# Optimization experiments

Measured on AMD Instinct MI355X. Metric: run time of the kernel, lower is better.

The kernel has to match this reference:

```python
import jax, jax.numpy as jnp
import numpy as np

BS, TS, H = 16, 2048, 1024
MT_LEN = TS // 2  # static split point; matches first_sentence_mask built in setup_inputs
SCALE = 1.0 / float(np.sqrt(H))
NEG = -10000.0


def masked_average(x, mask):
    # x: (bs, ts, h), mask: (bs, ts) -> (bs, h)
    m = mask[..., None].astype(x.dtype)
    return (x * m).sum(1) / m.sum(1)


def setup_inputs() -> dict:
    key = jax.random.key(0)
    ks = jax.random.split(key, 8)
    hidden_states = jax.random.normal(ks[0], (BS, TS, H), jnp.float32)
    embeddings = jax.random.normal(ks[1], (BS, TS, H), jnp.float32)
    attention_mask = jnp.ones((BS, TS), jnp.int32)
    first_sentence_mask = jnp.concatenate(
        [jnp.ones((BS, MT_LEN), jnp.int32), jnp.zeros((BS, TS - MT_LEN), jnp.int32)], axis=1)
    first_piece_mask = jnp.ones((BS, TS), jnp.int32)  # unused (aggregation='none')
    s = 1.0 / float(np.sqrt(H))
    Wq = jax.random.normal(ks[2], (H, H), jnp.float32) * s
    bq = jnp.zeros((H,), jnp.float32)
    Wk = jax.random.normal(ks[3], (H, H), jnp.float32) * s
    bk = jnp.zeros((H,), jnp.float32)
    Wv = jax.random.normal(ks[4], (H, H), jnp.float32) * s
    bv = jnp.zeros((H,), jnp.float32)
    return dict(hidden_states=hidden_states, embeddings=embeddings,
                attention_mask=attention_mask, first_sentence_mask=first_sentence_mask,
                first_piece_mask=first_piece_mask,
                Wq=Wq, bq=bq, Wk=Wk, bk=bk, Wv=Wv, bv=bv)


def reference(hidden_states, embeddings, attention_mask, first_sentence_mask,
              first_piece_mask, Wq, bq, Wk, bk, Wv, bv):
    # alpha_merge < 0, squared_attn=False, kv_rep='embeddings', alpha=1.0 (softmax)
    kv_rep = embeddings
    hidden_states_avg = masked_average(hidden_states, attention_mask)   # (bs, h)
    q = hidden_states_avg @ Wq.T + bq                                   # (bs, h)
    k = kv_rep @ Wk.T + bk                                              # (bs, ts, h)
    v = kv_rep @ Wv.T + bv                                              # (bs, ts, h)
    scores = jnp.einsum('bh,bth->bt', q, k) * SCALE                     # (bs, ts)
    scores = jnp.where(attention_mask.astype(bool), scores, NEG)
    probas = jax.nn.softmax(scores, axis=-1)                            # (bs, ts)
    combined_summary = jnp.einsum('bt,bth->bh', probas, v)              # (bs, h)
    # separate_mt_and_src on probas (static split at MT_LEN)
    mt_mask = attention_mask[:, :MT_LEN] * first_sentence_mask[:, :MT_LEN]
    src_mask = attention_mask[:, MT_LEN:] * (1 - first_sentence_mask[:, MT_LEN:])
    mt_probas = probas[:, :MT_LEN] * mt_mask.astype(probas.dtype)
    src_probas = probas[:, MT_LEN:] * src_mask.astype(probas.dtype)
    return combined_summary, mt_probas, src_probas
```

## Files before the change

kernel.cpp:

```cpp
#include <hip/hip_runtime.h>

#define BS 16
#define TS 2048
#define H 1024
#define MT_LEN 1024
#define NCHUNK 64
#define CHUNK_T (TS / NCHUNK)
#define SCALE 0.03125f
#define NEG -10000.0f

__global__ __launch_bounds__(256)
void k1_hidden_partial(const float* __restrict__ hs,
                       const int* __restrict__ am,
                       float* __restrict__ pA) {
    const int c = blockIdx.x, b = blockIdx.y;
    const int tid = threadIdx.x;
    const int h4 = tid * 4;
    __shared__ float ms[CHUNK_T];
    if (tid < CHUNK_T) ms[tid] = (float)am[b * TS + c * CHUNK_T + tid];
    __syncthreads();
    const float* base = hs + ((size_t)(b * TS + c * CHUNK_T)) * H + h4;
    float4 acc = {0.f, 0.f, 0.f, 0.f};
#pragma unroll 4
    for (int t = 0; t < CHUNK_T; ++t) {
        const float m = ms[t];
        float4 v = *(const float4*)(base + (size_t)t * H);
        acc.x += m * v.x; acc.y += m * v.y; acc.z += m * v.z; acc.w += m * v.w;
    }
    *(float4*)(pA + ((size_t)(b * NCHUNK + c)) * H + h4) = acc;
}

__global__ __launch_bounds__(256)
void k2_avg(const float* __restrict__ pA, const int* __restrict__ am,
            float* __restrict__ avg) {
    const int b = blockIdx.x;
    const int tid = threadIdx.x;
    __shared__ float red[256];
    int s = 0;
    for (int t = tid; t < TS; t += 256) s += am[b * TS + t];
    red[tid] = (float)s;
    __syncthreads();
    for (int o = 128; o > 0; o >>= 1) { if (tid < o) red[tid] += red[tid + o]; __syncthreads(); }
    const float inv = 1.0f / red[0];
    const int h4 = tid * 4;
    float4 acc = {0.f, 0.f, 0.f, 0.f};
    for (int c = 0; c < NCHUNK; ++c) {
        float4 v = *(const float4*)(pA + ((size_t)(b * NCHUNK + c)) * H + h4);
        acc.x += v.x; acc.y += v.y; acc.z += v.z; acc.w += v.w;
    }
    acc.x *= inv; acc.y *= inv; acc.z *= inv; acc.w *= inv;
    *(float4*)(avg + (size_t)b * H + h4) = acc;
}

__global__ __launch_bounds__(256)
void k3_q(const float* __restrict__ avg, const float* __restrict__ Wq,
          const float* __restrict__ bq, float* __restrict__ q) {
    const int b = blockIdx.y;
    const int tid = threadIdx.x;
    __shared__ float avs[H];
    *(float4*)(&avs[tid * 4]) = *(const float4*)(avg + (size_t)b * H + tid * 4);
    __syncthreads();
    const int wave = tid >> 6, lane = tid & 63;
    const int i = blockIdx.x * 4 + wave;
    const float* row = Wq + (size_t)i * H;
    float acc = 0.f;
#pragma unroll
    for (int u = 0; u < 4; ++u) {
        const int j = u * 256 + lane * 4;
        float4 w = *(const float4*)(row + j);
        float4 a = *(const float4*)(&avs[j]);
        acc += w.x * a.x + w.y * a.y + w.z * a.z + w.w * a.w;
    }
#pragma unroll
    for (int o = 32; o > 0; o >>= 1) acc += __shfl_xor(acc, o);
    if (lane == 0) q[b * H + i] = acc + bq[i];
}

__global__ __launch_bounds__(256)
void k4_qkp(const float* __restrict__ q, const float* __restrict__ Wk,
            const float* __restrict__ bk, float* __restrict__ qk_p,
            float* __restrict__ qbk_p) {
    const int ic = blockIdx.x, b = blockIdx.y;
    const int tid = threadIdx.x;
    __shared__ float qs[256];
    __shared__ float red[256];
    qs[tid] = q[b * H + ic * 256 + tid];
    __syncthreads();
    const int j = tid * 4;
    float4 acc = {0.f, 0.f, 0.f, 0.f};
#pragma unroll 8
    for (int ii = 0; ii < 256; ++ii) {
        const float s = qs[ii];
        float4 w = *(const float4*)(Wk + ((size_t)(ic * 256 + ii)) * H + j);
        acc.x += s * w.x; acc.y += s * w.y; acc.z += s * w.z; acc.w += s * w.w;
    }
    *(float4*)(qk_p + ((size_t)(ic * BS + b)) * H + j) = acc;
    red[tid] = qs[tid] * bk[ic * 256 + tid];
    __syncthreads();
    for (int o = 128; o > 0; o >>= 1) { if (tid < o) red[tid] += red[tid + o]; __syncthreads(); }
    if (tid == 0) qbk_p[ic * BS + b] = red[0];
}

__global__ __launch_bounds__(256)
void k5_fused(const float* __restrict__ emb, const int* __restrict__ am,
              const float* __restrict__ qk_p, const float* __restrict__ qbk_p,
              float* __restrict__ scores, float* __restrict__ mc_arr,
              float* __restrict__ zc_arr, float* __restrict__ e_c) {
    const int c = blockIdx.x, b = blockIdx.y;
    const int tid = threadIdx.x;
    __shared__ float qks[H];
    __shared__ float sbuf[CHUNK_T];
    __shared__ float wbuf[CHUNK_T];
    {
        const int j = tid * 4;
        float4 a = {0.f, 0.f, 0.f, 0.f};
#pragma unroll
        for (int ic = 0; ic < 4; ++ic) {
            float4 v = *(const float4*)(qk_p + ((size_t)(ic * BS + b)) * H + j);
            a.x += v.x; a.y += v.y; a.z += v.z; a.w += v.w;
        }
        *(float4*)(&qks[j]) = a;
    }
    const float qb = qbk_p[0 * BS + b] + qbk_p[1 * BS + b] + qbk_p[2 * BS + b] + qbk_p[3 * BS + b];
    __syncthreads();
    const int wave = tid >> 6, lane = tid & 63;
    for (int tt = 0; tt < 8; ++tt) {
        const int tl = wave * 8 + tt;
        const int t = c * CHUNK_T + tl;
        const float* e = emb + ((size_t)(b * TS + t)) * H;
        float acc = 0.f;
#pragma unroll
        for (int u = 0; u < 4; ++u) {
            const int j = u * 256 + lane * 4;
            float4 v = *(const float4*)(e + j);
            float4 a = *(const float4*)(&qks[j]);
            acc += v.x * a.x + v.y * a.y + v.z * a.z + v.w * a.w;
        }
#pragma unroll
        for (int o = 32; o > 0; o >>= 1) acc += __shfl_xor(acc, o);
        if (lane == 0) {
            const float sc = (am[b * TS + t] != 0) ? (acc + qb) * SCALE : NEG;
            scores[b * TS + t] = sc;
            sbuf[tl] = sc;
        }
    }
    __syncthreads();
    float mc = -3.4e38f;
#pragma unroll
    for (int tl = 0; tl < CHUNK_T; ++tl) mc = fmaxf(mc, sbuf[tl]);
    if (tid < CHUNK_T) wbuf[tid] = __expf(sbuf[tid] - mc);
    __syncthreads();
    float zc = 0.f;
#pragma unroll
    for (int tl = 0; tl < CHUNK_T; ++tl) zc += wbuf[tl];
    const int h4 = tid * 4;
    const float* base = emb + ((size_t)(b * TS + c * CHUNK_T)) * H + h4;
    float4 acc = {0.f, 0.f, 0.f, 0.f};
#pragma unroll 4
    for (int t = 0; t < CHUNK_T; ++t) {
        const float p = wbuf[t];
        float4 v = *(const float4*)(base + (size_t)t * H);
        acc.x += p * v.x; acc.y += p * v.y; acc.z += p * v.z; acc.w += p * v.w;
    }
    *(float4*)(e_c + ((size_t)(b * NCHUNK + c)) * H + h4) = acc;
    if (tid == 0) { mc_arr[b * NCHUNK + c] = mc; zc_arr[b * NCHUNK + c] = zc; }
}

__global__ __launch_bounds__(256)
void k6_combine(const float* __restrict__ mc_arr, const float* __restrict__ zc_arr,
                const float* __restrict__ e_c, float* __restrict__ e_comb,
                float* __restrict__ mz) {
    const int b = blockIdx.x;
    const int tid = threadIdx.x;
    __shared__ float mcs[NCHUNK], zcs[NCHUNK], scs[NCHUNK];
    if (tid < NCHUNK) { mcs[tid] = mc_arr[b * NCHUNK + tid]; zcs[tid] = zc_arr[b * NCHUNK + tid]; }
    __syncthreads();
    float m = -3.4e38f;
    for (int c = 0; c < NCHUNK; ++c) m = fmaxf(m, mcs[c]);
    float Z = 0.f;
    for (int c = 0; c < NCHUNK; ++c) Z += zcs[c] * __expf(mcs[c] - m);
    if (tid < NCHUNK) scs[tid] = __expf(mcs[tid] - m);
    __syncthreads();
    const float invZ = 1.0f / Z;
    const int h4 = tid * 4;
    float4 acc = {0.f, 0.f, 0.f, 0.f};
    for (int c = 0; c < NCHUNK; ++c) {
        const float s = scs[c];
        float4 v = *(const float4*)(e_c + ((size_t)(b * NCHUNK + c)) * H + h4);
        acc.x += s * v.x; acc.y += s * v.y; acc.z += s * v.z; acc.w += s * v.w;
    }
    acc.x *= invZ; acc.y *= invZ; acc.z *= invZ; acc.w *= invZ;
    *(float4*)(e_comb + (size_t)b * H + h4) = acc;
    if (tid == 0) { mz[b * 2] = m; mz[b * 2 + 1] = invZ; }
}

__global__ __launch_bounds__(256)
void k7_probas(const float* __restrict__ scores, const float* __restrict__ mz,
               const int* __restrict__ am, const int* __restrict__ fs,
               float* __restrict__ out) {
    const int b = blockIdx.x;
    const int tid = threadIdx.x;
    const float m = mz[b * 2], invZ = mz[b * 2 + 1];
#pragma unroll
    for (int u = 0; u < 8; ++u) {
        const int t = tid + u * 256;
        const float p = __expf(scores[b * TS + t] - m) * invZ;
        const int a = am[b * TS + t];
        const int f = fs[b * TS + t];
        if (t < MT_LEN)
            out[BS * H + b * MT_LEN + t] = p * (float)(a * f);
        else
            out[BS * H + BS * MT_LEN + b * (TS - MT_LEN) + (t - MT_LEN)] = p * (float)(a * (1 - f));
    }
}

__global__ __launch_bounds__(256)
void k8_out(const float* __restrict__ e_comb, const float* __restrict__ Wv,
            const float* __restrict__ bv, float* __restrict__ out) {
    const int b = blockIdx.y;
    const int tid = threadIdx.x;
    __shared__ float es[H];
    *(float4*)(&es[tid * 4]) = *(const float4*)(e_comb + (size_t)b * H + tid * 4);
    __syncthreads();
    const int wave = tid >> 6, lane = tid & 63;
    const int i = blockIdx.x * 4 + wave;
    const float* row = Wv + (size_t)i * H;
    float acc = 0.f;
#pragma unroll
    for (int u = 0; u < 4; ++u) {
        const int j = u * 256 + lane * 4;
        float4 w = *(const float4*)(row + j);
        float4 a = *(const float4*)(&es[j]);
        acc += w.x * a.x + w.y * a.y + w.z * a.z + w.w * a.w;
    }
#pragma unroll
    for (int o = 32; o > 0; o >>= 1) acc += __shfl_xor(acc, o);
    if (lane == 0) out[b * H + i] = acc + bv[i];
}

extern "C" void kernel_launch(void* const* d_in, const int* in_sizes, int n_in,
                              void* d_out, int out_size, void* d_ws, size_t ws_size,
                              hipStream_t stream) {
    const float* hs  = (const float*)d_in[0];
    const float* emb = (const float*)d_in[1];
    const int*   am  = (const int*)d_in[2];
    const int*   fs  = (const int*)d_in[3];
    const float* Wq  = (const float*)d_in[5];
    const float* bq  = (const float*)d_in[6];
    const float* Wk  = (const float*)d_in[7];
    const float* bk  = (const float*)d_in[8];
    const float* Wv  = (const float*)d_in[9];
    const float* bv  = (const float*)d_in[10];
    float* out = (float*)d_out;
    float* ws  = (float*)d_ws;

    float* pA     = ws;
    float* avg    = ws + 1048576;
    float* q      = ws + 1064960;
    float* qk_p   = ws + 1081344;
    float* qbk_p  = ws + 1146880;
    float* scores = ws + 1147136;
    float* mc_arr = ws + 1179904;
    float* zc_arr = ws + 1180928;
    float* e_c    = ws + 1181952;
    float* mz     = ws + 2230528;
    float* e_comb = ws + 2230784;

    k1_hidden_partial<<<dim3(NCHUNK, BS), 256, 0, stream>>>(hs, am, pA);
    k2_avg<<<BS, 256, 0, stream>>>(pA, am, avg);
    k3_q<<<dim3(H / 4, BS), 256, 0, stream>>>(avg, Wq, bq, q);
    k4_qkp<<<dim3(4, BS), 256, 0, stream>>>(q, Wk, bk, qk_p, qbk_p);
    k5_fused<<<dim3(NCHUNK, BS), 256, 0, stream>>>(emb, am, qk_p, qbk_p,
                                                   scores, mc_arr, zc_arr, e_c);
    k6_combine<<<BS, 256, 0, stream>>>(mc_arr, zc_arr, e_c, e_comb, mz);
    k7_probas<<<BS, 256, 0, stream>>>(scores, mz, am, fs, out);
    k8_out<<<dim3(H / 4, BS), 256, 0, stream>>>(e_comb, Wv, bv, out);
}
```

Baseline: 361.6 us.

## Stage embedding tile in LDS for single global read, double chunks, fuse combine+probas

```diff
diff --git a/kernel.cpp b/kernel.cpp
--- a/kernel.cpp
+++ b/kernel.cpp
@@ -6,6 +6,8 @@
 #define MT_LEN 1024
 #define NCHUNK 64
 #define CHUNK_T (TS / NCHUNK)
+#define NC5 128
+#define T5 (TS / NC5)
 #define SCALE 0.03125f
 #define NEG -10000.0f
 
@@ -109,8 +111,9 @@
     const int c = blockIdx.x, b = blockIdx.y;
     const int tid = threadIdx.x;
     __shared__ float qks[H];
-    __shared__ float sbuf[CHUNK_T];
-    __shared__ float wbuf[CHUNK_T];
+    __shared__ float ebuf[T5][H];
+    __shared__ float sbuf[T5];
+    __shared__ float wbuf[T5];
     {
         const int j = tid * 4;
         float4 a = {0.f, 0.f, 0.f, 0.f};
@@ -122,23 +125,28 @@
         *(float4*)(&qks[j]) = a;
     }
     const float qb = qbk_p[0 * BS + b] + qbk_p[1 * BS + b] + qbk_p[2 * BS + b] + qbk_p[3 * BS + b];
+    const float* src = emb + ((size_t)(b * TS + c * T5)) * H;
+#pragma unroll
+    for (int r = 0; r < T5; ++r) {
+        *(float4*)(&ebuf[r][tid * 4]) = *(const float4*)(src + (size_t)r * H + tid * 4);
+    }
     __syncthreads();
     const int wave = tid >> 6, lane = tid & 63;
-    for (int tt = 0; tt < 8; ++tt) {
-        const int tl = wave * 8 + tt;
-        const int t = c * CHUNK_T + tl;
-        const float* e = emb + ((size_t)(b * TS + t)) * H;
+    float4 qr[4];
+#pragma unroll
+    for (int u = 0; u < 4; ++u) qr[u] = *(const float4*)(&qks[u * 256 + lane * 4]);
+    for (int tt = 0; tt < 4; ++tt) {
+        const int tl = wave * 4 + tt;
         float acc = 0.f;
 #pragma unroll
         for (int u = 0; u < 4; ++u) {
-            const int j = u * 256 + lane * 4;
-            float4 v = *(const float4*)(e + j);
-            float4 a = *(const float4*)(&qks[j]);
-            acc += v.x * a.x + v.y * a.y + v.z * a.z + v.w * a.w;
+            float4 v = *(const float4*)(&ebuf[tl][u * 256 + lane * 4]);
+            acc += v.x * qr[u].x + v.y * qr[u].y + v.z * qr[u].z + v.w * qr[u].w;
         }
 #pragma unroll
         for (int o = 32; o > 0; o >>= 1) acc += __shfl_xor(acc, o);
         if (lane == 0) {
+            const int t = c * T5 + tl;
             const float sc = (am[b * TS + t] != 0) ? (acc + qb) * SCALE : NEG;
             scores[b * TS + t] = sc;
             sbuf[tl] = sc;
@@ -147,60 +155,50 @@
     __syncthreads();
     float mc = -3.4e38f;
 #pragma unroll
-    for (int tl = 0; tl < CHUNK_T; ++tl) mc = fmaxf(mc, sbuf[tl]);
-    if (tid < CHUNK_T) wbuf[tid] = __expf(sbuf[tid] - mc);
+    for (int tl = 0; tl < T5; ++tl) mc = fmaxf(mc, sbuf[tl]);
+    if (tid < T5) wbuf[tid] = __expf(sbuf[tid] - mc);
     __syncthreads();
     float zc = 0.f;
 #pragma unroll
-    for (int tl = 0; tl < CHUNK_T; ++tl) zc += wbuf[tl];
-    const int h4 = tid * 4;
-    const float* base = emb + ((size_t)(b * TS + c * CHUNK_T)) * H + h4;
-    float4 acc = {0.f, 0.f, 0.f, 0.f};
-#pragma unroll 4
-    for (int t = 0; t < CHUNK_T; ++t) {
+    for (int tl = 0; tl < T5; ++tl) zc += wbuf[tl];
+    const int h4 = tid * 4;
+    float4 acc = {0.f, 0.f, 0.f, 0.f};
+#pragma unroll
+    for (int t = 0; t < T5; ++t) {
         const float p = wbuf[t];
-        float4 v = *(const float4*)(base + (size_t)t * H);
+        float4 v = *(const float4*)(&ebuf[t][h4]);
         acc.x += p * v.x; acc.y += p * v.y; acc.z += p * v.z; acc.w += p * v.w;
     }
-    *(float4*)(e_c + ((size_t)(b * NCHUNK + c)) * H + h4) = acc;
-    if (tid == 0) { mc_arr[b * NCHUNK + c] = mc; zc_arr[b * NCHUNK + c] = zc; }
-}
-
-__global__ __launch_bounds__(256)
-void k6_combine(const float* __restrict__ mc_arr, const float* __restrict__ zc_arr,
-                const float* __restrict__ e_c, float* __restrict__ e_comb,
-                float* __restrict__ mz) {
+    *(float4*)(e_c + ((size_t)(b * NC5 + c)) * H + h4) = acc;
+    if (tid == 0) { mc_arr[b * NC5 + c] = mc; zc_arr[b * NC5 + c] = zc; }
+}
+
+__global__ __launch_bounds__(256)
+void k6_finish(const float* __restrict__ mc_arr, const float* __restrict__ zc_arr,
+               const float* __restrict__ e_c, const float* __restrict__ scores,
+               const int* __restrict__ am, const int* __restrict__ fs,
+               float* __restrict__ e_comb, float* __restrict__ out) {
     const int b = blockIdx.x;
     const int tid = threadIdx.x;
-    __shared__ float mcs[NCHUNK], zcs[NCHUNK], scs[NCHUNK];
-    if (tid < NCHUNK) { mcs[tid] = mc_arr[b * NCHUNK + tid]; zcs[tid] = zc_arr[b * NCHUNK + tid]; }
+    __shared__ float mcs[NC5], zcs[NC5], scs[NC5];
+    if (tid < NC5) { mcs[tid] = mc_arr[b * NC5 + tid]; zcs[tid] = zc_arr[b * NC5 + tid]; }
     __syncthreads();
     float m = -3.4e38f;
-    for (int c = 0; c < NCHUNK; ++c) m = fmaxf(m, mcs[c]);
+    for (int c = 0; c < NC5; ++c) m = fmaxf(m, mcs[c]);
     float Z = 0.f;
-    for (int c = 0; c < NCHUNK; ++c) Z += zcs[c] * __expf(mcs[c] - m);
-    if (tid < NCHUNK) scs[tid] = __expf(mcs[tid] - m);
+    for (int c = 0; c < NC5; ++c) Z += zcs[c] * __expf(mcs[c] - m);
+    if (tid < NC5) scs[tid] = __expf(mcs[tid] - m);
     __syncthreads();
     const float invZ = 1.0f / Z;
     const int h4 = tid * 4;
     float4 acc = {0.f, 0.f, 0.f, 0.f};
-    for (int c = 0; c < NCHUNK; ++c) {
+    for (int c = 0; c < NC5; ++c) {
         const float s = scs[c];
-        float4 v = *(const float4*)(e_c + ((size_t)(b * NCHUNK + c)) * H + h4);
+        float4 v = *(const float4*)(e_c + ((size_t)(b * NC5 + c)) * H + h4);
         acc.x += s * v.x; acc.y += s * v.y; acc.z += s * v.z; acc.w += s * v.w;
     }
     acc.x *= invZ; acc.y *= invZ; acc.z *= invZ; acc.w *= invZ;
     *(float4*)(e_comb + (size_t)b * H + h4) = acc;
-    if (tid == 0) { mz[b * 2] = m; mz[b * 2 + 1] = invZ; }
-}
-
-__global__ __launch_bounds__(256)
-void k7_probas(const float* __restrict__ scores, const float* __restrict__ mz,
-               const int* __restrict__ am, const int* __restrict__ fs,
-               float* __restrict__ out) {
-    const int b = blockIdx.x;
-    const int tid = threadIdx.x;
-    const float m = mz[b * 2], invZ = mz[b * 2 + 1];
 #pragma unroll
     for (int u = 0; u < 8; ++u) {
         const int t = tid + u * 256;
@@ -261,18 +259,16 @@
     float* qbk_p  = ws + 1146880;
     float* scores = ws + 1147136;
     float* mc_arr = ws + 1179904;
-    float* zc_arr = ws + 1180928;
-    float* e_c    = ws + 1181952;
-    float* mz     = ws + 2230528;
-    float* e_comb = ws + 2230784;
+    float* zc_arr = ws + 1181952;
+    float* e_c    = ws + 1184000;
+    float* e_comb = ws + 3281152;
 
     k1_hidden_partial<<<dim3(NCHUNK, BS), 256, 0, stream>>>(hs, am, pA);
     k2_avg<<<BS, 256, 0, stream>>>(pA, am, avg);
     k3_q<<<dim3(H / 4, BS), 256, 0, stream>>>(avg, Wq, bq, q);
     k4_qkp<<<dim3(4, BS), 256, 0, stream>>>(q, Wk, bk, qk_p, qbk_p);
-    k5_fused<<<dim3(NCHUNK, BS), 256, 0, stream>>>(emb, am, qk_p, qbk_p,
-                                                   scores, mc_arr, zc_arr, e_c);
-    k6_combine<<<BS, 256, 0, stream>>>(mc_arr, zc_arr, e_c, e_comb, mz);
-    k7_probas<<<BS, 256, 0, stream>>>(scores, mz, am, fs, out);
+    k5_fused<<<dim3(NC5, BS), 256, 0, stream>>>(emb, am, qk_p, qbk_p,
+                                                scores, mc_arr, zc_arr, e_c);
+    k6_finish<<<BS, 256, 0, stream>>>(mc_arr, zc_arr, e_c, scores, am, fs, e_comb, out);
     k8_out<<<dim3(H / 4, BS), 256, 0, stream>>>(e_comb, Wv, bv, out);
 }
```

Result: faster. 354.0 us (-2.1%).
